# Kernel optimization log

Hardware: AMD Instinct MI355X
Metric: run time of the kernel (lower is better)

## Reference

```python
import jax, jax.numpy as jnp
import numpy as np

RENORM_PERIOD = 256
MAX_NORM = 100.0


def setup_inputs() -> dict:
    key = jax.random.key(0)
    ks = jax.random.split(key, 9)
    B, S, G, D, N = 4, 2048, 8, 128, 64
    return {
        "x_r": jax.random.normal(ks[0], (B, S, G, D), jnp.float32),
        "x_i": jax.random.normal(ks[1], (B, S, G, D), jnp.float32),
        "log_A_mag": jax.random.uniform(ks[2], (G, N), jnp.float32) * 0.5 + 0.5,
        "A_phase": jax.random.normal(ks[3], (G, N), jnp.float32) * 0.1,
        "Bw_r": jax.random.normal(ks[4], (N, D), jnp.float32) / np.sqrt(D),
        "Bw_i": jax.random.normal(ks[5], (N, D), jnp.float32) / np.sqrt(D),
        "Cw_r": jax.random.normal(ks[6], (D, N), jnp.float32) / np.sqrt(N),
        "Cw_i": jax.random.normal(ks[7], (D, N), jnp.float32) / np.sqrt(N),
        "dt_w": jax.random.normal(ks[8], (2, 2 * D), jnp.float32) * 0.02,
        "dt_b": jnp.zeros((2,), jnp.float32),
    }


def reference(x_r, x_i, log_A_mag, A_phase, Bw_r, Bw_i, Cw_r, Cw_i, dt_w, dt_b):
    B, S, G, D = x_r.shape
    N = Bw_r.shape[0]
    # dt: input-dependent step magnitude / phase scale, clamped
    x_cat = jnp.concatenate([x_r, x_i], axis=-1)            # [B,S,G,2D]
    dt = jnp.clip(jnp.exp(jnp.einsum('bsgd,od->bsgo', x_cat, dt_w) + dt_b), 1e-4, 2.0)
    dt_mag = dt[..., 0:1]                                    # [B,S,G,1]
    dt_phase = dt[..., 1:2]
    # A_bar in polar form, |A| = exp(-softplus(log_A_mag)*dt_mag) < 1
    neg_log_A = -jax.nn.softplus(log_A_mag)[None, None]      # [1,1,G,N]
    A_mag = jnp.exp(dt_mag * neg_log_A)                      # [B,S,G,N]
    A_ang = dt_phase * A_phase[None, None]
    A_r = A_mag * jnp.cos(A_ang)
    A_i = A_mag * jnp.sin(A_ang)
    # Bx = (B_proj @ x) * dt_mag, complex linear
    Bx_r = (jnp.einsum('bsgd,nd->bsgn', x_r, Bw_r) - jnp.einsum('bsgd,nd->bsgn', x_i, Bw_i)) * dt_mag
    Bx_i = (jnp.einsum('bsgd,nd->bsgn', x_r, Bw_i) + jnp.einsum('bsgd,nd->bsgn', x_i, Bw_r)) * dt_mag

    def step(carry, inp):
        h_r, h_i = carry
        ar, ai, br, bi, t = inp
        nh_r = ar * h_r - ai * h_i + br
        nh_i = ar * h_i + ai * h_r + bi
        renorm = ((t + 1) % RENORM_PERIOD) == 0
        norm = jnp.sqrt(nh_r * nh_r + nh_i * nh_i + 1e-8)
        scale = jnp.minimum(norm, MAX_NORM) / norm
        nh_r = jnp.where(renorm, nh_r * scale, nh_r)
        nh_i = jnp.where(renorm, nh_i * scale, nh_i)
        return (nh_r, nh_i), (nh_r, nh_i)

    h0 = (jnp.zeros((B, G, N), jnp.float32), jnp.zeros((B, G, N), jnp.float32))
    xs = (jnp.moveaxis(A_r, 1, 0), jnp.moveaxis(A_i, 1, 0),
          jnp.moveaxis(Bx_r, 1, 0), jnp.moveaxis(Bx_i, 1, 0),
          jnp.arange(S))
    _, (all_h_r, all_h_i) = jax.lax.scan(step, h0, xs)       # [S,B,G,N]
    all_h_r = jnp.moveaxis(all_h_r, 0, 1)                    # [B,S,G,N]
    all_h_i = jnp.moveaxis(all_h_i, 0, 1)
    # y = C_proj(h), complex linear N -> D
    y_r = jnp.einsum('bsgn,dn->bsgd', all_h_r, Cw_r) - jnp.einsum('bsgn,dn->bsgd', all_h_i, Cw_i)
    y_i = jnp.einsum('bsgn,dn->bsgd', all_h_r, Cw_i) + jnp.einsum('bsgn,dn->bsgd', all_h_i, Cw_r)
    return jnp.stack([y_r, y_i], axis=0)                     # [2,B,S,G,D]
```

## Files before the change

### kernel.cpp

```cpp
#include <hip/hip_runtime.h>
#include <math.h>

#define B_ 4
#define S_ 2048
#define G_ 8
#define D_ 128
#define N_ 64
#define ROWS (B_*S_*G_)
#define CH 64
#define CLEN 32
#define YOFF (ROWS*D_)

typedef short bf16x8 __attribute__((ext_vector_type(8)));
typedef float f32x4  __attribute__((ext_vector_type(4)));
#define MFMA16(a,b,c) __builtin_amdgcn_mfma_f32_16x16x32_bf16(a,b,c,0,0,0)

__device__ __forceinline__ unsigned short bf16_rtne(float f) {
    unsigned u = __float_as_uint(f);
    unsigned r = (u + 0x7FFFu + ((u >> 16) & 1u)) >> 16;
    return (unsigned short)r;
}
__device__ __forceinline__ void split_bf16(float f, unsigned short &hi, unsigned short &lo) {
    hi = bf16_rtne(f);
    float hif = __uint_as_float(((unsigned)hi) << 16);
    lo = bf16_rtne(f - hif);
}
__device__ __forceinline__ unsigned pk_bf16(float a, float b) {
    unsigned r;
    asm("v_cvt_pk_bf16_f32 %0, %1, %2" : "=v"(r) : "v"(a), "v"(b));
    return r;
}
__device__ __forceinline__ float dot4(float4 a, float4 b) {
    return fmaf(a.x,b.x, fmaf(a.y,b.y, fmaf(a.z,b.z, a.w*b.w)));
}

__global__ __launch_bounds__(256) void k_prep(
    const float* __restrict__ bwr, const float* __restrict__ bwi,
    const float* __restrict__ cwr, const float* __restrict__ cwi,
    unsigned short* __restrict__ wbhi, unsigned short* __restrict__ wblo,
    unsigned short* __restrict__ wchi)
{
    int tid = blockIdx.x * 256 + threadIdx.x;
    if (tid < 4096) {
        int f = tid;
        int lane = f & 63, ks = (f >> 6) & 7, nt = (f >> 9) & 1, w = f >> 10;
        int l15 = lane & 15, quad = lane >> 4;
        int n = w * 32 + nt * 16 + l15;
        int k0 = ks * 32 + quad * 8;
        const float* src; float sgn = 1.f;
        if (n < 64) {
            if (k0 < 128) src = bwr + n * 128 + k0;
            else        { src = bwi + n * 128 + (k0 - 128); sgn = -1.f; }
        } else {
            if (k0 < 128) src = bwi + (n - 64) * 128 + k0;
            else          src = bwr + (n - 64) * 128 + (k0 - 128);
        }
        float4 v0 = *(const float4*)src;
        float4 v1 = *(const float4*)(src + 4);
        float vv[8] = {v0.x,v0.y,v0.z,v0.w,v1.x,v1.y,v1.z,v1.w};
        unsigned short h[8], l[8];
        #pragma unroll
        for (int j = 0; j < 8; j++) split_bf16(vv[j] * sgn, h[j], l[j]);
        #pragma unroll
        for (int j = 0; j < 8; j++) { wbhi[f*8+j] = h[j]; wblo[f*8+j] = l[j]; }
    } else {
        int f = tid - 4096;
        int lane = f & 63, ks = (f >> 6) & 3, nt = (f >> 8) & 3, w = f >> 10;
        int l15 = lane & 15, quad = lane >> 4;
        int n = w * 64 + nt * 16 + l15;
        int d = (n < 128) ? n : (n - 128);
        int k0 = ks * 32 + quad * 8;
        unsigned short h[8];
        #pragma unroll
        for (int j = 0; j < 8; j++) {
            int k = k0 + j, col = k >> 1;
            float val;
            if (n < 128) val = (k & 1) ? -cwi[d * 64 + col] : cwr[d * 64 + col];
            else         val = (k & 1) ?  cwr[d * 64 + col] : cwi[d * 64 + col];
            unsigned short hh, hl; split_bf16(val, hh, hl);
            h[j] = hh;
        }
        #pragma unroll
        for (int j = 0; j < 8; j++) wchi[f*8+j] = h[j];
    }
}

#define LDK1 264
__global__ __launch_bounds__(256, 4) void k_g1(
    const float* __restrict__ xr, const float* __restrict__ xi,
    const float* __restrict__ dtw, const float* __restrict__ dtb,
    const float* __restrict__ logAm, const float* __restrict__ Aph,
    const unsigned short* __restrict__ wbhi,
    unsigned* __restrict__ bxp,
    float* __restrict__ dt_mag, float* __restrict__ dt_ph,
    float4* __restrict__ trans)
{
    __shared__ __align__(16) unsigned short Ahi[32 * LDK1];
    __shared__ float4 comb[192];
    __shared__ float dms[64], dps[64];
    float* bxs = (float*)Ahi;
    const int t = threadIdx.x;
    const int lane = t & 63, w = t >> 6;
    const int l15 = lane & 15, quad = lane >> 4;
    const int bg = blockIdx.x >> 5, cp = blockIdx.x & 31;
    const int g = bg & 7, b = bg >> 3;
    const int c0 = cp * 2;

    const int kq = t & 31, k4 = kq * 4;
    float4 w0r = *(const float4*)(dtw + k4);
    float4 w0i = *(const float4*)(dtw + 128 + k4);
    float4 w1r = *(const float4*)(dtw + 256 + k4);
    float4 w1i = *(const float4*)(dtw + 384 + k4);
    float b0 = dtb[0], b1 = dtb[1];
    float nla = -logf(1.0f + __expf(logAm[g * N_ + lane]));
    float aph = Aph[g * N_ + lane];

    const bf16x8* WHp = (const bf16x8*)wbhi + (w * 2) * 512 + lane;

    const float* xrb = xr + ((size_t)(b * S_ + c0 * CLEN) * G_ + g) * 128;
    const float* xib = xi + ((size_t)(b * S_ + c0 * CLEN) * G_ + g) * 128;

    float4 XA[2][4], XB[2][4];
    #pragma unroll
    for (int q = 0; q < 2; q++)
        #pragma unroll
        for (int i = 0; i < 4; i++) {
            int f = t + 256 * i;
            int m = f >> 5, kk = f & 31;
            XA[q][i] = ((const float4*)(xrb + q * 32768 + m * 1024))[kk];
            XB[q][i] = ((const float4*)(xib + q * 32768 + m * 1024))[kk];
        }

    #pragma unroll 1
    for (int q = 0; q < 2; q++) {
        __syncthreads();
        const int c = c0 + q;
        const int crow = (bg * CH + c) * CLEN;
        bf16x8 wh0 = WHp[0];
        bf16x8 wh1 = WHp[512];

        float pm[4], pp[4];
        #pragma unroll
        for (int i = 0; i < 4; i++) {
            int f = t + 256 * i;
            int m = f >> 5, kk = f & 31;
            float4 a  = XA[q][i];
            float4 bb = XB[q][i];
            *(uint2*)&Ahi[m * LDK1 + kk * 4] =
                make_uint2(pk_bf16(a.x, a.y), pk_bf16(a.z, a.w));
            *(uint2*)&Ahi[m * LDK1 + 128 + kk * 4] =
                make_uint2(pk_bf16(bb.x, bb.y), pk_bf16(bb.z, bb.w));
            pm[i] = dot4(a, w0r) + dot4(bb, w0i);
            pp[i] = dot4(a, w1r) + dot4(bb, w1i);
        }
        #pragma unroll
        for (int i = 0; i < 4; i++) {
            float vm = pm[i], vp = pp[i];
            #pragma unroll
            for (int msk = 16; msk >= 1; msk >>= 1) {
                vm += __shfl_xor(vm, msk);
                vp += __shfl_xor(vp, msk);
            }
            if ((t & 31) == 0) {
                int m = (t >> 5) + 8 * i;
                float dm = fminf(fmaxf(__expf(vm + b0), 1e-4f), 2.0f);
                float dp = fminf(fmaxf(__expf(vp + b1), 1e-4f), 2.0f);
                dms[q * 32 + m] = dm; dps[q * 32 + m] = dp;
                dt_mag[crow + m] = dm; dt_ph[crow + m] = dp;
            }
        }
        __syncthreads();

        f32x4 acc[2][2];
        #pragma unroll
        for (int a = 0; a < 2; a++)
            #pragma unroll
            for (int bq = 0; bq < 2; bq++)
                acc[a][bq] = (f32x4){0.f, 0.f, 0.f, 0.f};
        #pragma unroll
        for (int ks = 0; ks < 8; ks++) {
            bf16x8 nh0, nh1;
            if (ks < 7) {
                nh0 = WHp[(ks + 1) * 64];
                nh1 = WHp[512 + (ks + 1) * 64];
            }
            #pragma unroll
            for (int ms = 0; ms < 2; ms++) {
                int arow = (ms * 16 + l15) * LDK1 + quad * 8;
                bf16x8 ah = *(const bf16x8*)&Ahi[arow + ks * 32];
                acc[ms][0] = MFMA16(ah, wh0, acc[ms][0]);
                acc[ms][1] = MFMA16(ah, wh1, acc[ms][1]);
            }
            if (ks < 7) { wh0 = nh0; wh1 = nh1; }
        }
        __syncthreads();

        #pragma unroll
        for (int ms = 0; ms < 2; ms++)
            #pragma unroll
            for (int nt = 0; nt < 2; nt++) {
                int n = w * 32 + nt * 16 + l15;
                #pragma unroll
                for (int r = 0; r < 4; r++) {
                    int m = ms * 16 + quad * 4 + r;
                    bxs[m * 132 + n] = acc[ms][nt][r] * dms[q * 32 + m];
                }
            }
        __syncthreads();

        #pragma unroll
        for (int i = 0; i < 8; i++) {
            int e = t + 256 * i;
            int m = e >> 6, n = e & 63;
            unsigned u = pk_bf16(bxs[m * 132 + n], bxs[m * 132 + 64 + n]);
            bxp[(crow + m) * 64 + n] = u;
        }
        {
            float Ar = 1.f, Ai = 0.f, Br = 0.f, Bi = 0.f;
            const int base = w * 8;
            #pragma unroll
            for (int tt = 0; tt < 8; tt++) {
                const int m = base + tt;
                float dm = dms[q * 32 + m], dp = dps[q * 32 + m];
                float am  = __expf(dm * nla);
                float ang = dp * aph;
                float cr = am * __cosf(ang), ci = am * __sinf(ang);
                float vr = bxs[m * 132 + lane], vi = bxs[m * 132 + 64 + lane];
                float nAr = cr * Ar - ci * Ai;
                float nAi = cr * Ai + ci * Ar;
                float nBr = cr * Br - ci * Bi + vr;
                float nBi = cr * Bi + ci * Br + vi;
                Ar = nAr; Ai = nAi; Br = nBr; Bi = nBi;
            }
            if (w < 3) comb[w * 64 + lane] = make_float4(Ar, Ai, Br, Bi);
            __syncthreads();
            if (w == 3) {
                float4 cc0 = comb[lane];
                float cAr = cc0.x, cAi = cc0.y, cBr = cc0.z, cBi = cc0.w;
                #pragma unroll
                for (int s = 1; s < 3; s++) {
                    float4 ps = comb[s * 64 + lane];
                    float nAr = ps.x * cAr - ps.y * cAi;
                    float nAi = ps.x * cAi + ps.y * cAr;
                    float nBr = ps.x * cBr - ps.y * cBi + ps.z;
                    float nBi = ps.x * cBi + ps.y * cBr + ps.w;
                    cAr = nAr; cAi = nAi; cBr = nBr; cBi = nBi;
                }
                float fAr = Ar * cAr - Ai * cAi;
                float fAi = Ar * cAi + Ai * cAr;
                float fBr = Ar * cBr - Ai * cBi + Br;
                float fBi = Ar * cBi + Ai * cBr + Bi;
                trans[(bg * CH + c) * 64 + lane] = make_float4(fAr, fAi, fBr, fBi);
            }
        }
    }
}

__global__ __launch_bounds__(256) void k_scanB2(const float4* __restrict__ trans,
    float2* __restrict__ hstart)
{
    int w = threadIdx.x >> 6, lane = threadIdx.x & 63;
    int W = blockIdx.x * 4 + w;
    int bg = W >> 3;
    int n  = ((W & 7) << 3) + (lane & 7);
    int j  = lane >> 3;
    float pAr[8], pAi[8], pBr[8], pBi[8];
    float Ar = 1.f, Ai = 0.f, Br = 0.f, Bi = 0.f;
    const float4* tp = trans + (bg * CH + j * 8) * 64 + n;
    #pragma unroll
    for (int k = 0; k < 8; k++) {
        pAr[k] = Ar; pAi[k] = Ai; pBr[k] = Br; pBi[k] = Bi;
        float4 T = tp[k * 64];
        float nAr = T.x * Ar - T.y * Ai;
        float nAi = T.x * Ai + T.y * Ar;
        float nBr = T.x * Br - T.y * Bi + T.z;
        float nBi = T.x * Bi + T.y * Br + T.w;
        Ar = nAr; Ai = nAi; Br = nBr; Bi = nBi;
    }
    float hr = 0.f, hi = 0.f, mhr = 0.f, mhi = 0.f;
    #pragma unroll
    for (int j2 = 0; j2 < 8; j2++) {
        if (j2 == j) { mhr = hr; mhi = hi; }
        int src = j2 * 8 + (lane & 7);
        float sAr = __shfl(Ar, src), sAi = __shfl(Ai, src);
        float sBr = __shfl(Br, src), sBi = __shfl(Bi, src);
        float nr = sAr * hr - sAi * hi + sBr;
        float ni = sAr * hi + sAi * hr + sBi;
        float nrm = sqrtf(nr * nr + ni * ni + 1e-8f);
        float sc = fminf(nrm, 100.f) / nrm;
        hr = nr * sc; hi = ni * sc;
    }
    float2* hp = hstart + (bg * CH + j * 8) * 64 + n;
    #pragma unroll
    for (int k = 0; k < 8; k++) {
        float hsr = pAr[k] * mhr - pAi[k] * mhi + pBr[k];
        float hsi = pAr[k] * mhi + pAi[k] * mhr + pBi[k];
        hp[k * 64] = make_float2(hsr, hsi);
    }
}

#define LDK2 152
__global__ __launch_bounds__(256, 6) void k_sg4(
    const unsigned* __restrict__ bxp,
    const float* __restrict__ dt_mag, const float* __restrict__ dt_ph,
    const float* __restrict__ logAm, const float* __restrict__ Aph,
    const float2* __restrict__ hstart,
    const unsigned short* __restrict__ wchi,
    float* __restrict__ out)
{
    __shared__ __align__(16) unsigned short Ahi[32 * LDK2];
    __shared__ __align__(16) unsigned short Alo[32 * LDK2];
    __shared__ float4 comb[256];
    const int t = threadIdx.x;
    const int lane = t & 63, w = t >> 6;
    const int l15 = lane & 15, quad = lane >> 4;
    const int bg = blockIdx.x >> 6, c = blockIdx.x & 63;
    const int g = bg & 7, b = bg >> 3;
    const int base = (bg * CH + c) * CLEN;
    const int s8 = w * 8;

    unsigned bxv[8];
    #pragma unroll
    for (int s = 0; s < 8; s++)
        bxv[s] = bxp[(base + s8 + s) * 64 + lane];
    float dval = 0.f;
    if (lane < 8)       dval = dt_mag[base + s8 + lane];
    else if (lane < 16) dval = dt_ph[base + s8 + (lane - 8)];
    float2 h0 = hstart[(bg * CH + c) * 64 + lane];
    float nla = -logf(1.0f + __expf(logAm[g * N_ + lane]));
    float aph = Aph[g * N_ + lane];

    float paR[8], paI[8], pbR[8], pbI[8];
    {
        float Ar = 1.f, Ai = 0.f, Br = 0.f, Bi = 0.f;
        #pragma unroll
        for (int s = 0; s < 8; s++) {
            float dm = __shfl(dval, s), dp = __shfl(dval, 8 + s);
            float am  = __expf(dm * nla);
            float ang = dp * aph;
            float cr = am * __cosf(ang), ci = am * __sinf(ang);
            unsigned u = bxv[s];
            float vr = __uint_as_float(u << 16);
            float vi = __uint_as_float(u & 0xFFFF0000u);
            float nAr = cr * Ar - ci * Ai;
            float nAi = cr * Ai + ci * Ar;
            float nBr = cr * Br - ci * Bi + vr;
            float nBi = cr * Bi + ci * Br + vi;
            Ar = nAr; Ai = nAi; Br = nBr; Bi = nBi;
            paR[s] = Ar; paI[s] = Ai; pbR[s] = Br; pbI[s] = Bi;
        }
        comb[w * 64 + lane] = make_float4(Ar, Ai, Br, Bi);
    }
    __syncthreads();

    float Hr = h0.x, Hi = h0.y;
    for (int s2 = 0; s2 < w; s2++) {
        float4 T = comb[s2 * 64 + lane];
        float nr = T.x * Hr - T.y * Hi + T.z;
        float ni = T.x * Hi + T.y * Hr + T.w;
        Hr = nr; Hi = ni;
    }
    {
        const bool rn = ((c & 7) == 7) && (w == 3);
        #pragma unroll
        for (int s = 0; s < 8; s++) {
            float hr = paR[s] * Hr - paI[s] * Hi + pbR[s];
            float hi = paR[s] * Hi + paI[s] * Hr + pbI[s];
            if (rn && s == 7) {
                float nrm = sqrtf(hr * hr + hi * hi + 1e-8f);
                float scale = fminf(nrm, 100.0f) / nrm;
                hr *= scale; hi *= scale;
            }
            unsigned hp = pk_bf16(hr, hi);
            float rr = hr - __uint_as_float(hp << 16);
            float ri = hi - __uint_as_float(hp & 0xFFFF0000u);
            unsigned lp = pk_bf16(rr, ri);
            int tt = s8 + s;
            *(unsigned*)&Ahi[tt * LDK2 + 2 * lane] = hp;
            *(unsigned*)&Alo[tt * LDK2 + 2 * lane] = lp;
        }
    }
    __syncthreads();

    f32x4 acc[2][4];
    #pragma unroll
    for (int a = 0; a < 2; a++)
        #pragma unroll
        for (int bq = 0; bq < 4; bq++)
            acc[a][bq] = (f32x4){0.f, 0.f, 0.f, 0.f};
    #pragma unroll
    for (int ks = 0; ks < 4; ks++) {
        bf16x8 wc0 = ((const bf16x8*)wchi)[((w * 4 + 0) * 4 + ks) * 64 + lane];
        bf16x8 wc1 = ((const bf16x8*)wchi)[((w * 4 + 1) * 4 + ks) * 64 + lane];
        bf16x8 wc2 = ((const bf16x8*)wchi)[((w * 4 + 2) * 4 + ks) * 64 + lane];
        bf16x8 wc3 = ((const bf16x8*)wchi)[((w * 4 + 3) * 4 + ks) * 64 + lane];
        #pragma unroll
        for (int ms = 0; ms < 2; ms++) {
            int arow = (ms * 16 + l15) * LDK2 + quad * 8;
            bf16x8 ah = *(const bf16x8*)&Ahi[arow + ks * 32];
            bf16x8 al = *(const bf16x8*)&Alo[arow + ks * 32];
            acc[ms][0] = MFMA16(al, wc0, acc[ms][0]);
            acc[ms][0] = MFMA16(ah, wc0, acc[ms][0]);
            acc[ms][1] = MFMA16(al, wc1, acc[ms][1]);
            acc[ms][1] = MFMA16(ah, wc1, acc[ms][1]);
            acc[ms][2] = MFMA16(al, wc2, acc[ms][2]);
            acc[ms][2] = MFMA16(ah, wc2, acc[ms][2]);
            acc[ms][3] = MFMA16(al, wc3, acc[ms][3]);
            acc[ms][3] = MFMA16(ah, wc3, acc[ms][3]);
        }
    }
    #pragma unroll
    for (int ms = 0; ms < 2; ms++)
        #pragma unroll
        for (int nt = 0; nt < 4; nt++) {
            int nn = w * 64 + nt * 16 + l15;
            float* dst = (nn < 128) ? (out + nn) : (out + YOFF + (nn - 128));
            #pragma unroll
            for (int r = 0; r < 4; r++) {
                int tt2 = ms * 16 + quad * 4 + r;
                int srow = (b * S_ + c * CLEN + tt2) * G_ + g;
                dst[srow * 128] = acc[ms][nt][r];
            }
        }
}

extern "C" void kernel_launch(void* const* d_in, const int* in_sizes, int n_in,
                              void* d_out, int out_size, void* d_ws, size_t ws_size,
                              hipStream_t stream) {
    (void)in_sizes; (void)n_in; (void)out_size; (void)ws_size;
    const float* xr    = (const float*)d_in[0];
    const float* xi    = (const float*)d_in[1];
    const float* logAm = (const float*)d_in[2];
    const float* Aph   = (const float*)d_in[3];
    const float* bwr   = (const float*)d_in[4];
    const float* bwi   = (const float*)d_in[5];
    const float* cwr   = (const float*)d_in[6];
    const float* cwi   = (const float*)d_in[7];
    const float* dtw   = (const float*)d_in[8];
    const float* dtb   = (const float*)d_in[9];
    float* out = (float*)d_out;
    float* ws  = (float*)d_ws;

    float*    dt_mag = ws;
    float*    dt_ph  = ws + 65536;
    unsigned* bxp    = (unsigned*)(ws + 131072);
    float4*   trans  = (float4*)(ws + 8519680);
    float2*   hstart = (float2*)(ws + 9043968);
    unsigned short* wbhi = (unsigned short*)(ws + 9306112);
    unsigned short* wblo = wbhi + 32768;
    unsigned short* wchi = wblo + 32768;

    hipLaunchKernelGGL(k_prep,   dim3(32), dim3(256), 0, stream,
                       bwr, bwi, cwr, cwi, wbhi, wblo, wchi);
    hipLaunchKernelGGL(k_g1,     dim3((B_ * G_) * 32), dim3(256), 0, stream,
                       xr, xi, dtw, dtb, logAm, Aph, wbhi,
                       bxp, dt_mag, dt_ph, trans);
    hipLaunchKernelGGL(k_scanB2, dim3(64), dim3(256), 0, stream,
                       trans, hstart);
    hipLaunchKernelGGL(k_sg4,    dim3((B_ * G_) * 64), dim3(256), 0, stream,
                       bxp, dt_mag, dt_ph, logAm, Aph, hstart, wchi, out);
}
```

Baseline: 187.1 us.

## Split k_g1 to one chunk per block and stage k_sg4 output through LDS

k_g1 now handles one chunk per block instead of two, using twice as many blocks and a higher occupancy hint. This drops the register-held prefetch of both chunks' inputs. k_sg4 now writes its MFMA accumulators to shared memory and stores the output as coalesced 16-byte row vectors, replacing the strided scalar stores. The cost is extra LDS traffic and barriers in k_sg4, and k_g1 loses the overlap from prefetching the second chunk.

```diff
diff --git a/kernel.cpp b/kernel.cpp
--- a/kernel.cpp
+++ b/kernel.cpp
@@ -86,7 +86,7 @@
 }
 
 #define LDK1 264
-__global__ __launch_bounds__(256, 4) void k_g1(
+__global__ __launch_bounds__(256, 8) void k_g1(
     const float* __restrict__ xr, const float* __restrict__ xi,
     const float* __restrict__ dtw, const float* __restrict__ dtb,
     const float* __restrict__ logAm, const float* __restrict__ Aph,
@@ -97,14 +97,14 @@
 {
     __shared__ __align__(16) unsigned short Ahi[32 * LDK1];
     __shared__ float4 comb[192];
-    __shared__ float dms[64], dps[64];
+    __shared__ float dms[32], dps[32];
     float* bxs = (float*)Ahi;
     const int t = threadIdx.x;
     const int lane = t & 63, w = t >> 6;
     const int l15 = lane & 15, quad = lane >> 4;
-    const int bg = blockIdx.x >> 5, cp = blockIdx.x & 31;
+    const int bg = blockIdx.x >> 6, c = blockIdx.x & 63;
     const int g = bg & 7, b = bg >> 3;
-    const int c0 = cp * 2;
+    const int crow = (bg * CH + c) * CLEN;
 
     const int kq = t & 31, k4 = kq * 4;
     float4 w0r = *(const float4*)(dtw + k4);
@@ -116,142 +116,123 @@
     float aph = Aph[g * N_ + lane];
 
     const bf16x8* WHp = (const bf16x8*)wbhi + (w * 2) * 512 + lane;
-
-    const float* xrb = xr + ((size_t)(b * S_ + c0 * CLEN) * G_ + g) * 128;
-    const float* xib = xi + ((size_t)(b * S_ + c0 * CLEN) * G_ + g) * 128;
-
-    float4 XA[2][4], XB[2][4];
-    #pragma unroll
-    for (int q = 0; q < 2; q++)
-        #pragma unroll
-        for (int i = 0; i < 4; i++) {
-            int f = t + 256 * i;
-            int m = f >> 5, kk = f & 31;
-            XA[q][i] = ((const float4*)(xrb + q * 32768 + m * 1024))[kk];
-            XB[q][i] = ((const float4*)(xib + q * 32768 + m * 1024))[kk];
-        }
-
-    #pragma unroll 1
-    for (int q = 0; q < 2; q++) {
+    bf16x8 wh0 = WHp[0];
+    bf16x8 wh1 = WHp[512];
+
+    const float* xrb = xr + ((size_t)(b * S_ + c * CLEN) * G_ + g) * 128;
+    const float* xib = xi + ((size_t)(b * S_ + c * CLEN) * G_ + g) * 128;
+
+    float pm[4], pp[4];
+    #pragma unroll
+    for (int i = 0; i < 4; i++) {
+        int f = t + 256 * i;
+        int m = f >> 5, kk = f & 31;
+        float4 a  = ((const float4*)(xrb + m * 1024))[kk];
+        float4 bb = ((const float4*)(xib + m * 1024))[kk];
+        *(uint2*)&Ahi[m * LDK1 + kk * 4] =
+            make_uint2(pk_bf16(a.x, a.y), pk_bf16(a.z, a.w));
+        *(uint2*)&Ahi[m * LDK1 + 128 + kk * 4] =
+            make_uint2(pk_bf16(bb.x, bb.y), pk_bf16(bb.z, bb.w));
+        pm[i] = dot4(a, w0r) + dot4(bb, w0i);
+        pp[i] = dot4(a, w1r) + dot4(bb, w1i);
+    }
+    #pragma unroll
+    for (int i = 0; i < 4; i++) {
+        float vm = pm[i], vp = pp[i];
+        #pragma unroll
+        for (int msk = 16; msk >= 1; msk >>= 1) {
+            vm += __shfl_xor(vm, msk);
+            vp += __shfl_xor(vp, msk);
+        }
+        if ((t & 31) == 0) {
+            int m = (t >> 5) + 8 * i;
+            float dm = fminf(fmaxf(__expf(vm + b0), 1e-4f), 2.0f);
+            float dp = fminf(fmaxf(__expf(vp + b1), 1e-4f), 2.0f);
+            dms[m] = dm; dps[m] = dp;
+            dt_mag[crow + m] = dm; dt_ph[crow + m] = dp;
+        }
+    }
+    __syncthreads();
+
+    f32x4 acc[2][2];
+    #pragma unroll
+    for (int a = 0; a < 2; a++)
+        #pragma unroll
+        for (int bq = 0; bq < 2; bq++)
+            acc[a][bq] = (f32x4){0.f, 0.f, 0.f, 0.f};
+    #pragma unroll
+    for (int ks = 0; ks < 8; ks++) {
+        bf16x8 nh0, nh1;
+        if (ks < 7) {
+            nh0 = WHp[(ks + 1) * 64];
+            nh1 = WHp[512 + (ks + 1) * 64];
+        }
+        #pragma unroll
+        for (int ms = 0; ms < 2; ms++) {
+            int arow = (ms * 16 + l15) * LDK1 + quad * 8;
+            bf16x8 ah = *(const bf16x8*)&Ahi[arow + ks * 32];
+            acc[ms][0] = MFMA16(ah, wh0, acc[ms][0]);
+            acc[ms][1] = MFMA16(ah, wh1, acc[ms][1]);
+        }
+        if (ks < 7) { wh0 = nh0; wh1 = nh1; }
+    }
+    __syncthreads();
+
+    #pragma unroll
+    for (int ms = 0; ms < 2; ms++)
+        #pragma unroll
+        for (int nt = 0; nt < 2; nt++) {
+            int n = w * 32 + nt * 16 + l15;
+            #pragma unroll
+            for (int r = 0; r < 4; r++) {
+                int m = ms * 16 + quad * 4 + r;
+                bxs[m * 132 + n] = acc[ms][nt][r] * dms[m];
+            }
+        }
+    __syncthreads();
+
+    #pragma unroll
+    for (int i = 0; i < 8; i++) {
+        int e = t + 256 * i;
+        int m = e >> 6, n = e & 63;
+        bxp[(crow + m) * 64 + n] = pk_bf16(bxs[m * 132 + n], bxs[m * 132 + 64 + n]);
+    }
+    {
+        float Ar = 1.f, Ai = 0.f, Br = 0.f, Bi = 0.f;
+        const int base = w * 8;
+        #pragma unroll
+        for (int tt = 0; tt < 8; tt++) {
+            const int m = base + tt;
+            float dm = dms[m], dp = dps[m];
+            float am  = __expf(dm * nla);
+            float ang = dp * aph;
+            float cr = am * __cosf(ang), ci = am * __sinf(ang);
+            float vr = bxs[m * 132 + lane], vi = bxs[m * 132 + 64 + lane];
+            float nAr = cr * Ar - ci * Ai;
+            float nAi = cr * Ai + ci * Ar;
+            float nBr = cr * Br - ci * Bi + vr;
+            float nBi = cr * Bi + ci * Br + vi;
+            Ar = nAr; Ai = nAi; Br = nBr; Bi = nBi;
+        }
+        if (w < 3) comb[w * 64 + lane] = make_float4(Ar, Ai, Br, Bi);
         __syncthreads();
-        const int c = c0 + q;
-        const int crow = (bg * CH + c) * CLEN;
-        bf16x8 wh0 = WHp[0];
-        bf16x8 wh1 = WHp[512];
-
-        float pm[4], pp[4];
-        #pragma unroll
-        for (int i = 0; i < 4; i++) {
-            int f = t + 256 * i;
-            int m = f >> 5, kk = f & 31;
-            float4 a  = XA[q][i];
-            float4 bb = XB[q][i];
-            *(uint2*)&Ahi[m * LDK1 + kk * 4] =
-                make_uint2(pk_bf16(a.x, a.y), pk_bf16(a.z, a.w));
-            *(uint2*)&Ahi[m * LDK1 + 128 + kk * 4] =
-                make_uint2(pk_bf16(bb.x, bb.y), pk_bf16(bb.z, bb.w));
-            pm[i] = dot4(a, w0r) + dot4(bb, w0i);
-            pp[i] = dot4(a, w1r) + dot4(bb, w1i);
-        }
-        #pragma unroll
-        for (int i = 0; i < 4; i++) {
-            float vm = pm[i], vp = pp[i];
+        if (w == 3) {
+            float4 cc0 = comb[lane];
+            float cAr = cc0.x, cAi = cc0.y, cBr = cc0.z, cBi = cc0.w;
             #pragma unroll
-            for (int msk = 16; msk >= 1; msk >>= 1) {
-                vm += __shfl_xor(vm, msk);
-                vp += __shfl_xor(vp, msk);
+            for (int s = 1; s < 3; s++) {
+                float4 ps = comb[s * 64 + lane];
+                float nAr = ps.x * cAr - ps.y * cAi;
+                float nAi = ps.x * cAi + ps.y * cAr;
+                float nBr = ps.x * cBr - ps.y * cBi + ps.z;
+                float nBi = ps.x * cBi + ps.y * cBr + ps.w;
+                cAr = nAr; cAi = nAi; cBr = nBr; cBi = nBi;
             }
-            if ((t & 31) == 0) {
-                int m = (t >> 5) + 8 * i;
-                float dm = fminf(fmaxf(__expf(vm + b0), 1e-4f), 2.0f);
-                float dp = fminf(fmaxf(__expf(vp + b1), 1e-4f), 2.0f);
-                dms[q * 32 + m] = dm; dps[q * 32 + m] = dp;
-                dt_mag[crow + m] = dm; dt_ph[crow + m] = dp;
-            }
-        }
-        __syncthreads();
-
-        f32x4 acc[2][2];
-        #pragma unroll
-        for (int a = 0; a < 2; a++)
-            #pragma unroll
-            for (int bq = 0; bq < 2; bq++)
-                acc[a][bq] = (f32x4){0.f, 0.f, 0.f, 0.f};
-        #pragma unroll
-        for (int ks = 0; ks < 8; ks++) {
-            bf16x8 nh0, nh1;
-            if (ks < 7) {
-                nh0 = WHp[(ks + 1) * 64];
-                nh1 = WHp[512 + (ks + 1) * 64];
-            }
-            #pragma unroll
-            for (int ms = 0; ms < 2; ms++) {
-                int arow = (ms * 16 + l15) * LDK1 + quad * 8;
-                bf16x8 ah = *(const bf16x8*)&Ahi[arow + ks * 32];
-                acc[ms][0] = MFMA16(ah, wh0, acc[ms][0]);
-                acc[ms][1] = MFMA16(ah, wh1, acc[ms][1]);
-            }
-            if (ks < 7) { wh0 = nh0; wh1 = nh1; }
-        }
-        __syncthreads();
-
-        #pragma unroll
-        for (int ms = 0; ms < 2; ms++)
-            #pragma unroll
-            for (int nt = 0; nt < 2; nt++) {
-                int n = w * 32 + nt * 16 + l15;
-                #pragma unroll
-                for (int r = 0; r < 4; r++) {
-                    int m = ms * 16 + quad * 4 + r;
-                    bxs[m * 132 + n] = acc[ms][nt][r] * dms[q * 32 + m];
-                }
-            }
-        __syncthreads();
-
-        #pragma unroll
-        for (int i = 0; i < 8; i++) {
-            int e = t + 256 * i;
-            int m = e >> 6, n = e & 63;
-            unsigned u = pk_bf16(bxs[m * 132 + n], bxs[m * 132 + 64 + n]);
-            bxp[(crow + m) * 64 + n] = u;
-        }
-        {
-            float Ar = 1.f, Ai = 0.f, Br = 0.f, Bi = 0.f;
-            const int base = w * 8;
-            #pragma unroll
-            for (int tt = 0; tt < 8; tt++) {
-                const int m = base + tt;
-                float dm = dms[q * 32 + m], dp = dps[q * 32 + m];
-                float am  = __expf(dm * nla);
-                float ang = dp * aph;
-                float cr = am * __cosf(ang), ci = am * __sinf(ang);
-                float vr = bxs[m * 132 + lane], vi = bxs[m * 132 + 64 + lane];
-                float nAr = cr * Ar - ci * Ai;
-                float nAi = cr * Ai + ci * Ar;
-                float nBr = cr * Br - ci * Bi + vr;
-                float nBi = cr * Bi + ci * Br + vi;
-                Ar = nAr; Ai = nAi; Br = nBr; Bi = nBi;
-            }
-            if (w < 3) comb[w * 64 + lane] = make_float4(Ar, Ai, Br, Bi);
-            __syncthreads();
-            if (w == 3) {
-                float4 cc0 = comb[lane];
-                float cAr = cc0.x, cAi = cc0.y, cBr = cc0.z, cBi = cc0.w;
-                #pragma unroll
-                for (int s = 1; s < 3; s++) {
-                    float4 ps = comb[s * 64 + lane];
-                    float nAr = ps.x * cAr - ps.y * cAi;
-                    float nAi = ps.x * cAi + ps.y * cAr;
-                    float nBr = ps.x * cBr - ps.y * cBi + ps.z;
-                    float nBi = ps.x * cBi + ps.y * cBr + ps.w;
-                    cAr = nAr; cAi = nAi; cBr = nBr; cBi = nBi;
-                }
-                float fAr = Ar * cAr - Ai * cAi;
-                float fAi = Ar * cAi + Ai * cAr;
-                float fBr = Ar * cBr - Ai * cBi + Br;
-                float fBi = Ar * cBi + Ai * cBr + Bi;
-                trans[(bg * CH + c) * 64 + lane] = make_float4(fAr, fAi, fBr, fBi);
-            }
+            float fAr = Ar * cAr - Ai * cAi;
+            float fAi = Ar * cAi + Ai * cAr;
+            float fBr = Ar * cBr - Ai * cBi + Br;
+            float fBi = Ar * cBi + Ai * cBr + Bi;
+            trans[(bg * CH + c) * 64 + lane] = make_float4(fAr, fAi, fBr, fBi);
         }
     }
 }
@@ -300,6 +281,7 @@
 }
 
 #define LDK2 152
+#define OTS 260
 __global__ __launch_bounds__(256, 6) void k_sg4(
     const unsigned* __restrict__ bxp,
     const float* __restrict__ dt_mag, const float* __restrict__ dt_ph,
@@ -311,6 +293,7 @@
     __shared__ __align__(16) unsigned short Ahi[32 * LDK2];
     __shared__ __align__(16) unsigned short Alo[32 * LDK2];
     __shared__ float4 comb[256];
+    float* OT = (float*)Ahi;
     const int t = threadIdx.x;
     const int lane = t & 63, w = t >> 6;
     const int l15 = lane & 15, quad = lane >> 4;
@@ -409,19 +392,28 @@
             acc[ms][3] = MFMA16(ah, wc3, acc[ms][3]);
         }
     }
-    #pragma unroll
-    for (int ms = 0; ms < 2; ms++)
-        #pragma unroll
-        for (int nt = 0; nt < 4; nt++) {
-            int nn = w * 64 + nt * 16 + l15;
-            float* dst = (nn < 128) ? (out + nn) : (out + YOFF + (nn - 128));
+    __syncthreads();
+
+    #pragma unroll 1
+    for (int ms = 0; ms < 2; ms++) {
+        #pragma unroll
+        for (int nt = 0; nt < 4; nt++)
             #pragma unroll
-            for (int r = 0; r < 4; r++) {
-                int tt2 = ms * 16 + quad * 4 + r;
-                int srow = (b * S_ + c * CLEN + tt2) * G_ + g;
-                dst[srow * 128] = acc[ms][nt][r];
-            }
-        }
+            for (int r = 0; r < 4; r++)
+                OT[(quad * 4 + r) * OTS + w * 64 + nt * 16 + l15] = acc[ms][nt][r];
+        __syncthreads();
+        #pragma unroll
+        for (int jj = 0; jj < 4; jj++) {
+            int idx = t + 256 * jj;
+            int rl = idx >> 6, rem = idx & 63;
+            int plane = rem >> 5, c4 = rem & 31;
+            f32x4 v = *(const f32x4*)&OT[rl * OTS + plane * 128 + c4 * 4];
+            int srow = (b * S_ + c * CLEN + ms * 16 + rl) * G_ + g;
+            float* dst = (plane ? out + YOFF : out) + (size_t)srow * 128 + c4 * 4;
+            *(f32x4*)dst = v;
+        }
+        __syncthreads();
+    }
 }
 
 extern "C" void kernel_launch(void* const* d_in, const int* in_sizes, int n_in,
@@ -452,7 +444,7 @@
 
     hipLaunchKernelGGL(k_prep,   dim3(32), dim3(256), 0, stream,
                        bwr, bwi, cwr, cwi, wbhi, wblo, wchi);
-    hipLaunchKernelGGL(k_g1,     dim3((B_ * G_) * 32), dim3(256), 0, stream,
+    hipLaunchKernelGGL(k_g1,     dim3((B_ * G_) * 64), dim3(256), 0, stream,
                        xr, xi, dtw, dtb, logAm, Aph, wbhi,
                        bxp, dt_mag, dt_ph, trans);
     hipLaunchKernelGGL(k_scanB2, dim3(64), dim3(256), 0, stream,
```

Measured after the change: 199.7 us. 6.8% more time.
